# Performance work log

Hardware: AMD Instinct MI355X
Metric: run time of the kernel (lower is better)

Reference implementation:

```python
import jax, jax.numpy as jnp
import numpy as np

DIM = 1024
NUM_HEADS = 16
HEAD_DIM = DIM // NUM_HEADS
SCALE = HEAD_DIM ** -0.5


def setup_inputs() -> dict:
    key = jax.random.key(0)
    k1, k2, k3 = jax.random.split(key, 3)
    B, N = 2, 2048
    x = jax.random.normal(k1, (B, N, DIM), dtype=jnp.float32)
    W_qkv = jax.random.normal(k2, (DIM, 3 * DIM), dtype=jnp.float32) * (DIM ** -0.5)
    b_qkv = jnp.zeros((3 * DIM,), dtype=jnp.float32)
    W_proj = jax.random.normal(k3, (DIM, DIM), dtype=jnp.float32) * (DIM ** -0.5)
    b_proj = jnp.zeros((DIM,), dtype=jnp.float32)
    return {"x": x, "W_qkv": W_qkv, "b_qkv": b_qkv, "W_proj": W_proj, "b_proj": b_proj}


def reference(x, W_qkv, b_qkv, W_proj, b_proj):
    B, N, D = x.shape
    qkv = x @ W_qkv + b_qkv                      # [B, N, 3D]
    qkv = qkv.reshape(B, N, 3, NUM_HEADS, HEAD_DIM)
    qkv = jnp.transpose(qkv, (2, 0, 3, 1, 4))    # [3, B, H, N, hd]
    q, k, v = qkv[0], qkv[1], qkv[2]
    attn = jnp.einsum('bhqd,bhkd->bhqk', q, k) * SCALE  # [B, H, N, N]
    attn = jax.nn.softmax(attn, axis=-1)
    out = jnp.einsum('bhqk,bhkd->bhqd', attn, v)        # [B, H, N, hd]
    out = jnp.transpose(out, (0, 2, 1, 3)).reshape(B, N, D)
    out = out @ W_proj + b_proj
    return out
```

## Files before the change

### kernel.cpp

```cpp
#include <hip/hip_runtime.h>


typedef __bf16 bf16_t;
typedef __bf16 bf16x2 __attribute__((ext_vector_type(2)));
typedef __bf16 bf16x4 __attribute__((ext_vector_type(4)));
typedef __bf16 bf16x8 __attribute__((ext_vector_type(8)));
typedef float  f32x4  __attribute__((ext_vector_type(4)));

#define NTOK 2048
#define DIM  1024
#define NH   16
#define HD   64
#define SCL2 0.18033688011112042f

#define MFMA16(a, b, c) __builtin_amdgcn_mfma_f32_16x16x32_bf16((a), (b), (c), 0, 0, 0)

__device__ __forceinline__ void gload_lds16(const void* g, void* l) {
  __builtin_amdgcn_global_load_lds((const __attribute__((address_space(1))) void*)g,
                                   (__attribute__((address_space(3))) void*)l, 16, 0, 0);
}

__device__ __forceinline__ void transpose_cvt_tile(const float* __restrict__ W,
                                                   bf16_t* __restrict__ WT,
                                                   int cols, int bx, int by) {
  __shared__ float tile[32][33];
  int j0 = bx * 32, i0 = by * 32;
  int c = threadIdx.x & 31, r0 = threadIdx.x >> 5;
#pragma unroll
  for (int it = 0; it < 4; ++it) {
    int r = r0 + it * 8;
    tile[r][c] = W[(long)(i0 + r) * cols + j0 + c];
  }
  __syncthreads();
#pragma unroll
  for (int it = 0; it < 4; ++it) {
    int r = r0 + it * 8;
    int orow = j0 + r, ocol = i0 + c;
    WT[(long)orow * 1024 + ((((ocol >> 3) ^ (orow & 7)) << 3) | (ocol & 7))] =
        (bf16_t)tile[c][r];
  }
}

__global__ __launch_bounds__(256) void k_prep(const float* __restrict__ x,
                                              bf16_t* __restrict__ xb,
                                              const float* __restrict__ Wq,
                                              bf16_t* __restrict__ WqT,
                                              const float* __restrict__ Wp,
                                              bf16_t* __restrict__ WpT) {
  int id = blockIdx.x;
  if (id < 2048) {
    int i = (id * 256 + threadIdx.x) * 8;
    float4 a = *(const float4*)(x + i);
    float4 b = *(const float4*)(x + i + 4);
    bf16x8 v;
    v[0] = (bf16_t)a.x; v[1] = (bf16_t)a.y; v[2] = (bf16_t)a.z; v[3] = (bf16_t)a.w;
    v[4] = (bf16_t)b.x; v[5] = (bf16_t)b.y; v[6] = (bf16_t)b.z; v[7] = (bf16_t)b.w;
    int r = i >> 10, c = (i & 1023) >> 3;
    *(bf16x8*)(xb + r * 1024 + ((c ^ (r & 7)) << 3)) = v;
  } else if (id < 2048 + 3072) {
    int t = id - 2048;
    transpose_cvt_tile(Wq, WqT, 3072, t % 96, t / 96);
  } else {
    int t = id - 5120;
    transpose_cvt_tile(Wp, WpT, 1024, t & 31, t >> 5);
  }
}

__device__ __forceinline__ void gemm_core(const bf16_t* __restrict__ A,
                                          const bf16_t* __restrict__ B,
                                          int K, int bm, int bn,
                                          bf16_t* As, bf16_t* Bs, f32x4 acc[4][4]) {
  const int t = threadIdx.x;
  const int lane = t & 63;
  const int w = t >> 6;
  const int wr = (w >> 1) * 64, wc = (w & 1) * 64;
  const int l15 = lane & 15, g = lane >> 4;
  const int srow = t >> 3, scol = (t & 7) * 8;
  const f32x4 vzero = {0.f, 0.f, 0.f, 0.f};
#pragma unroll
  for (int m = 0; m < 4; ++m)
#pragma unroll
    for (int n = 0; n < 4; ++n) acc[m][n] = vzero;

  const bf16_t* ga = A + (long)(bm + srow) * K + scol;
  const bf16_t* gb = B + (long)(bn + srow) * K + scol;
  bf16_t* lA = As + srow * 64 + scol;
  bf16_t* lB = Bs + srow * 64 + scol;
  const int xr = l15 & 7;

  auto stageAB = [&](int buf, int k0) {
#pragma unroll
    for (int j = 0; j < 4; ++j) {
      gload_lds16(ga + (long)32 * j * K + k0, lA + buf * 8192 + j * 2048);
      gload_lds16(gb + (long)32 * j * K + k0, lB + buf * 8192 + j * 2048);
    }
  };

  stageAB(0, 0);
  __syncthreads();
  int cur = 0;

  for (int k0 = 0; k0 < K; k0 += 64) {
    if (k0 + 64 < K) stageAB(cur ^ 1, k0 + 64);
    const char* Ab = (const char*)(As + cur * 8192);
    const char* Bb = (const char*)(Bs + cur * 8192);
#pragma unroll
    for (int kk = 0; kk < 2; ++kk) {
      bf16x8 af[4], bfv[4];
#pragma unroll
      for (int m = 0; m < 4; ++m)
        af[m] = *(const bf16x8*)(Ab + (wr + m * 16 + l15) * 128 +
                                 (((kk * 4 + g) ^ xr) << 4));
#pragma unroll
      for (int n = 0; n < 4; ++n)
        bfv[n] = *(const bf16x8*)(Bb + (wc + n * 16 + l15) * 128 +
                                  (((kk * 4 + g) ^ xr) << 4));
#pragma unroll
      for (int m = 0; m < 4; ++m)
#pragma unroll
        for (int n = 0; n < 4; ++n)
          acc[m][n] = MFMA16(af[m], bfv[n], acc[m][n]);
    }
    __syncthreads();
    cur ^= 1;
  }
}

__global__ __launch_bounds__(256) void k_gemm_qkv(const bf16_t* __restrict__ xb,
                                                  const bf16_t* __restrict__ WqT,
                                                  const float* __restrict__ bq,
                                                  bf16_t* __restrict__ Qb,
                                                  bf16_t* __restrict__ Kb,
                                                  bf16_t* __restrict__ Vt) {
  __shared__ alignas(16) bf16_t As[2 * 128 * 64];
  __shared__ alignas(16) bf16_t Bs[2 * 128 * 64];
  f32x4 acc[4][4];
  const int bid = blockIdx.x;
  const int xcd = bid & 7, ib = bid >> 3;
  const int bn = (xcd * 3 + (ib >> 5)) * 128;
  const int bm = (ib & 31) * 128;
  gemm_core(xb, WqT, DIM, bm, bn, As, Bs, acc);

  const int lane = threadIdx.x & 63, w = threadIdx.x >> 6;
  const int wr = (w >> 1) * 64, wc = (w & 1) * 64;
  const int l15 = lane & 15, g = lane >> 4;
#pragma unroll
  for (int n = 0; n < 4; ++n) {
    int col = bn + wc + n * 16 + l15;
    float bias = bq[col];
    int t3 = col >> 10, rem = col & 1023;
    int h = rem >> 6, d = rem & 63;
#pragma unroll
    for (int m = 0; m < 4; ++m) {
      int rowb = bm + wr + m * 16 + g * 4;
#pragma unroll
      for (int r = 0; r < 4; ++r) {
        int row = rowb + r;
        int b = row >> 11, tok = row & 2047;
        int bh = b * NH + h;
        float val = acc[m][n][r] + bias;
        if (t3 == 0) {
          Qb[bh * (NTOK * HD) + tok * HD + d] = (bf16_t)(val * SCL2);
        } else if (t3 == 1) {
          int rr = tok & 63;
          int off = bh * (NTOK * HD) + (tok >> 6) * 4096 + rr * 64 +
                    (((d >> 3) ^ (rr & 7)) << 3) + (d & 7);
          Kb[off] = (bf16_t)val;
        } else {
          int ct = tok & 63;
          int off = bh * (NTOK * HD) + (tok >> 6) * 4096 + d * 64 +
                    (((ct >> 3) ^ (d & 7)) << 3) + (ct & 7);
          Vt[off] = (bf16_t)val;
        }
      }
    }
  }
}

__global__ __launch_bounds__(256, 3) void k_attn(const bf16_t* __restrict__ Qb,
                                                 const bf16_t* __restrict__ Kb,
                                                 const bf16_t* __restrict__ Vt,
                                                 bf16_t* __restrict__ Ob) {
  __shared__ alignas(16) bf16_t Ks[2][64 * 64];
  __shared__ alignas(16) bf16_t Vs[2][64 * 64];
  __shared__ alignas(16) char  P2[4][4096];

  const int b0 = blockIdx.x;
  const int swz = (b0 & 7) * 64 + (b0 >> 3);
  const int qt = swz & 15, bh = swz >> 4;
  const int b = bh >> 4, h = bh & 15;
  const int t = threadIdx.x;
  const int w = t >> 6, lane = t & 63;
  const int l15 = lane & 15, g = lane >> 4;
  const bf16_t* Qp = Qb + bh * (NTOK * HD);
  const bf16_t* Kp = Kb + bh * (NTOK * HD);
  const bf16_t* Vp = Vt + bh * (NTOK * HD);
  const int q0 = qt * 128 + w * 32;
  char* P2w = &P2[w][0];

  const int cs0 = ((g ^ (l15 & 7)) << 4);
  const int cs1 = cs0 ^ 64;

  bf16x8 qfr[2][2];
#pragma unroll
  for (int qf = 0; qf < 2; ++qf)
#pragma unroll
    for (int kk = 0; kk < 2; ++kk)
      qfr[qf][kk] = *(const bf16x8*)(Qp + (q0 + qf * 16 + l15) * HD + kk * 32 + g * 8);

  bf16x8 ones;
#pragma unroll
  for (int i = 0; i < 8; ++i) ones[i] = (bf16_t)1.0f;

  const f32x4 vzero = {0.f, 0.f, 0.f, 0.f};
  f32x4 o[2][4];
#pragma unroll
  for (int qf = 0; qf < 2; ++qf)
#pragma unroll
    for (int df = 0; df < 4; ++df) o[qf][df] = vzero;
  f32x4 o_sum[2] = {vzero, vzero};

  auto stage = [&](int buf, int tile) {
    const bf16_t* gk = Kp + tile * 4096 + t * 8;
    const bf16_t* gv = Vp + tile * 4096 + t * 8;
    gload_lds16(gk,        (char*)Ks[buf] + t * 16);
    gload_lds16(gk + 2048, (char*)Ks[buf] + 4096 + t * 16);
    gload_lds16(gv,        (char*)Vs[buf] + t * 16);
    gload_lds16(gv + 2048, (char*)Vs[buf] + 4096 + t * 16);
  };

  stage(0, 0);
  __syncthreads();
  int cur = 0;

  for (int kt = 0; kt < NTOK; kt += 64) {
    if (kt + 64 < NTOK) stage(cur ^ 1, (kt >> 6) + 1);
    const char* kbuf = (const char*)Ks[cur];
    const char* vbuf = (const char*)Vs[cur];
    f32x4 s[2][4];
    __builtin_amdgcn_s_setprio(1);
#pragma unroll
    for (int kf = 0; kf < 4; ++kf) {
      int rb = (kf * 16 + l15) * 128;
      bf16x8 ka0 = *(const bf16x8*)(kbuf + rb + cs0);
      bf16x8 ka1 = *(const bf16x8*)(kbuf + rb + cs1);
      s[0][kf] = MFMA16(ka0, qfr[0][0], vzero);
      s[1][kf] = MFMA16(ka0, qfr[1][0], vzero);
      s[0][kf] = MFMA16(ka1, qfr[0][1], s[0][kf]);
      s[1][kf] = MFMA16(ka1, qfr[1][1], s[1][kf]);
    }
    __builtin_amdgcn_s_setprio(0);
#pragma unroll
    for (int qf = 0; qf < 2; ++qf)
#pragma unroll
      for (int kf = 0; kf < 4; ++kf) {
        bf16x4 pw;
        pw[0] = (bf16_t)__builtin_amdgcn_exp2f(s[qf][kf][0]);
        pw[1] = (bf16_t)__builtin_amdgcn_exp2f(s[qf][kf][1]);
        pw[2] = (bf16_t)__builtin_amdgcn_exp2f(s[qf][kf][2]);
        pw[3] = (bf16_t)__builtin_amdgcn_exp2f(s[qf][kf][3]);
        *(bf16x4*)(P2w + qf * 2048 + (2 * kf + (g >> 1)) * 256 + l15 * 16 + 8 * (g & 1)) = pw;
      }
    __builtin_amdgcn_s_setprio(1);
#pragma unroll
    for (int kb = 0; kb < 2; ++kb) {
      bf16x8 pf0 = *(const bf16x8*)(P2w + kb * 1024 + lane * 16);
      bf16x8 pf1 = *(const bf16x8*)(P2w + 2048 + kb * 1024 + lane * 16);
      int csk = kb ? cs1 : cs0;
      o_sum[0] = MFMA16(ones, pf0, o_sum[0]);
      o_sum[1] = MFMA16(ones, pf1, o_sum[1]);
#pragma unroll
      for (int df = 0; df < 4; ++df) {
        bf16x8 va = *(const bf16x8*)(vbuf + (df * 16 + l15) * 128 + csk);
        o[0][df] = MFMA16(va, pf0, o[0][df]);
        o[1][df] = MFMA16(va, pf1, o[1][df]);
      }
    }
    __builtin_amdgcn_s_setprio(0);
    __syncthreads();
    cur ^= 1;
  }
#pragma unroll
  for (int qf = 0; qf < 2; ++qf) {
    float inv = 1.0f / o_sum[qf][0];
    int tok = q0 + qf * 16 + l15;
    bf16_t* oprow = Ob + (long)(b * NTOK + tok) * DIM;
    const int xr = l15 & 7;
#pragma unroll
    for (int df = 0; df < 4; ++df) {
#pragma unroll
      for (int rp = 0; rp < 2; ++rp) {
        bf16x2 v2;
        v2[0] = (bf16_t)(o[qf][df][rp * 2]     * inv);
        v2[1] = (bf16_t)(o[qf][df][rp * 2 + 1] * inv);
        int c = h * 8 + df * 2 + (g >> 1);
        *(bf16x2*)(oprow + ((c ^ xr) << 3) + (g & 1) * 4 + rp * 2) = v2;
      }
    }
  }
}

__global__ __launch_bounds__(256) void k_gemm_proj(const bf16_t* __restrict__ Ob,
                                                   const bf16_t* __restrict__ WpT,
                                                   const float* __restrict__ bp,
                                                   float* __restrict__ out) {
  __shared__ alignas(16) bf16_t As[2 * 128 * 64];
  __shared__ alignas(16) bf16_t Bs[2 * 128 * 64];
  f32x4 acc[4][4];
  const int bid = blockIdx.x;
  const int bn = (bid & 7) * 128;
  const int bm = (bid >> 3) * 128;
  gemm_core(Ob, WpT, DIM, bm, bn, As, Bs, acc);

  const int lane = threadIdx.x & 63, w = threadIdx.x >> 6;
  const int wr = (w >> 1) * 64, wc = (w & 1) * 64;
  const int l15 = lane & 15, g = lane >> 4;
#pragma unroll
  for (int n = 0; n < 4; ++n) {
    int col = bn + wc + n * 16 + l15;
    float bias = bp[col];
#pragma unroll
    for (int m = 0; m < 4; ++m) {
      int rowb = bm + wr + m * 16 + g * 4;
#pragma unroll
      for (int r = 0; r < 4; ++r)
        out[(long)(rowb + r) * DIM + col] = acc[m][n][r] + bias;
    }
  }
}

extern "C" void kernel_launch(void* const* d_in, const int* in_sizes, int n_in,
                              void* d_out, int out_size, void* d_ws, size_t ws_size,
                              hipStream_t stream) {
  const float* x     = (const float*)d_in[0];
  const float* Wqkv  = (const float*)d_in[1];
  const float* bqkv  = (const float*)d_in[2];
  const float* Wproj = (const float*)d_in[3];
  const float* bproj = (const float*)d_in[4];
  float* out = (float*)d_out;

  char* ws = (char*)d_ws;
  bf16_t* xb  = (bf16_t*)(ws);
  bf16_t* WqT = (bf16_t*)(ws + (8l  << 20));
  bf16_t* WpT = (bf16_t*)(ws + (14l << 20));
  bf16_t* Qb  = (bf16_t*)(ws + (16l << 20));
  bf16_t* Kb  = (bf16_t*)(ws + (24l << 20));
  bf16_t* Vt  = (bf16_t*)(ws + (32l << 20));
  bf16_t* Ob  = (bf16_t*)(ws);

  k_prep<<<6144, 256, 0, stream>>>(x, xb, Wqkv, WqT, Wproj, WpT);
  k_gemm_qkv<<<768, 256, 0, stream>>>(xb, WqT, bqkv, Qb, Kb, Vt);
  k_attn<<<512, 256, 0, stream>>>(Qb, Kb, Vt, Ob);
  k_gemm_proj<<<256, 256, 0, stream>>>(Ob, WpT, bproj, out);
}
```

Baseline: 119.5 us.

## Keep two loads in flight with partial vmcnt waits in GEMM and attention loops

Replaces the __syncthreads-based double buffering in the GEMM core and the attention loop with an explicit pipeline. Two tiles are prefetched up front, each iteration waits only for the older tile via a partial s_waitcnt vmcnt, and the refill into the freed buffer is issued after a trailing barrier. The goal is to stop draining all outstanding global->LDS loads every iteration so memory latency overlaps compute. It depends on exact vmcnt counting matching the number of loads per stage, and relies on the raw s_barrier plus inline asm waits for LDS ordering, which is fragile if the compiler reorders or inserts other loads.

```diff
diff --git a/kernel.cpp b/kernel.cpp
--- a/kernel.cpp
+++ b/kernel.cpp
@@ -96,14 +96,16 @@
     }
   };
 
+  const int nsteps = K >> 6;
   stageAB(0, 0);
-  __syncthreads();
-  int cur = 0;
-
-  for (int k0 = 0; k0 < K; k0 += 64) {
-    if (k0 + 64 < K) stageAB(cur ^ 1, k0 + 64);
-    const char* Ab = (const char*)(As + cur * 8192);
-    const char* Bb = (const char*)(Bs + cur * 8192);
+  stageAB(1, 64);
+
+  for (int s = 0; s < nsteps; ++s) {
+    if (s == nsteps - 1) asm volatile("s_waitcnt vmcnt(0)" ::: "memory");
+    else                 asm volatile("s_waitcnt vmcnt(8)" ::: "memory");
+    __builtin_amdgcn_s_barrier();
+    const char* Ab = (const char*)(As + (s & 1) * 8192);
+    const char* Bb = (const char*)(Bs + (s & 1) * 8192);
 #pragma unroll
     for (int kk = 0; kk < 2; ++kk) {
       bf16x8 af[4], bfv[4];
@@ -121,8 +123,8 @@
         for (int n = 0; n < 4; ++n)
           acc[m][n] = MFMA16(af[m], bfv[n], acc[m][n]);
     }
-    __syncthreads();
-    cur ^= 1;
+    __builtin_amdgcn_s_barrier();
+    if (s + 2 < nsteps) stageAB(s & 1, (s + 2) * 64);
   }
 }
 
@@ -230,13 +232,14 @@
   };
 
   stage(0, 0);
-  __syncthreads();
-  int cur = 0;
-
-  for (int kt = 0; kt < NTOK; kt += 64) {
-    if (kt + 64 < NTOK) stage(cur ^ 1, (kt >> 6) + 1);
-    const char* kbuf = (const char*)Ks[cur];
-    const char* vbuf = (const char*)Vs[cur];
+  stage(1, 1);
+
+  for (int i = 0; i < 32; ++i) {
+    if (i == 31) asm volatile("s_waitcnt vmcnt(0)" ::: "memory");
+    else         asm volatile("s_waitcnt vmcnt(4)" ::: "memory");
+    __builtin_amdgcn_s_barrier();
+    const char* kbuf = (const char*)Ks[i & 1];
+    const char* vbuf = (const char*)Vs[i & 1];
     f32x4 s[2][4];
     __builtin_amdgcn_s_setprio(1);
 #pragma unroll
@@ -277,8 +280,8 @@
       }
     }
     __builtin_amdgcn_s_setprio(0);
-    __syncthreads();
-    cur ^= 1;
+    __builtin_amdgcn_s_barrier();
+    if (i + 2 < 32) stage(i & 1, i + 2);
   }
 #pragma unroll
   for (int qf = 0; qf < 2; ++qf) {
```

Measured after the change: 121.1 us. Within noise of the previous version (+1.3%).
